# Performance work log

Hardware: AMD Instinct MI355X
Metric: run time of the kernel (lower is better)

The kernel has to match this reference:

```python
import jax, jax.numpy as jnp
import numpy as np

H = 256          # hidden_size
TH_X = 0.05      # delta threshold on inputs
TH_H = 0.05      # delta threshold on hidden state
F_IN = 6         # engineered feature count


def hardswish(v):
    return v * jnp.clip(v + 3.0, 0.0, 6.0) / 6.0


def setup_inputs() -> dict:
    key = jax.random.key(0)
    ks = jax.random.split(key, 6)
    B, T = 32, 4096
    x = jax.random.normal(ks[0], (B, T, 2), dtype=jnp.float32)
    # x2h: Linear(6, 3H, bias=False) -> weight (3H, 6)
    Wx = jax.random.normal(ks[1], (3 * H, F_IN), dtype=jnp.float32) * (1.0 / np.sqrt(F_IN))
    # h2h: Linear(H, 3H, bias=False) -> weight (3H, H)
    Wh = jax.random.normal(ks[2], (3 * H, H), dtype=jnp.float32) * (1.0 / np.sqrt(H))
    # fc_out: Linear(H, 2, bias=False)
    Wo = jax.random.normal(ks[3], (2, H), dtype=jnp.float32) * (1.0 / np.sqrt(H))
    # tcn conv1: Conv1d(2, 3, k=3, padding=16, dilation=16, bias=False) -> (O,I,K)=(3,2,3)
    Wc1 = jax.random.normal(ks[4], (3, 2, 3), dtype=jnp.float32) * 0.3
    # tcn conv2: Conv1d(3, 2, k=1) -> (2,3,1)
    Wc2 = jax.random.normal(ks[5], (2, 3, 1), dtype=jnp.float32) * 0.3
    return {"x": x, "Wx": Wx, "Wh": Wh, "Wo": Wo, "Wc1": Wc1, "Wc2": Wc2}


def _delta_gru(feats_TBF, Wx, Wh):
    # feats_TBF: (T, B, 6). Initial states are always zeros (the torch module
    # resets them whenever x_p_0 is None, which DeltaGRUModel always passes).
    T, B, F = feats_TBF.shape
    dt = feats_TBF.dtype
    carry0 = (
        jnp.zeros((B, F), dt),        # x_p
        jnp.zeros((B, H), dt),        # h
        jnp.zeros((B, H), dt),        # h_p
        jnp.zeros((B, H), dt),        # dm_nh
        jnp.zeros((B, 3 * H), dt),    # dm
    )

    def step(carry, xt):
        x_p, h, h_p, dm_nh, dm = carry
        dx = xt - x_p
        dh = h - h_p
        dxa = jnp.abs(dx)
        dha = jnp.abs(dh)
        dx = jnp.where(dxa < TH_X, 0.0, dx)
        dh = jnp.where(dha < TH_H, 0.0, dh)
        x_p = jnp.where(dxa >= TH_X, xt, x_p)
        h_p = jnp.where(dha >= TH_H, h, h_p)
        mac_x = dx @ Wx.T + dm          # (B, 3H)
        mac_h = dh @ Wh.T               # (B, 3H)
        mxr, mxz, mxn = jnp.split(mac_x, 3, axis=1)
        mhr, mhz, mhn = jnp.split(mac_h, 3, axis=1)
        dm_r = mxr + mhr
        dm_z = mxz + mhz
        dm_n = mxn
        dm_nh = mhn + dm_nh
        dm = jnp.concatenate([dm_r, dm_z, dm_n], axis=1)
        r = jax.nn.sigmoid(dm_r)
        z = jax.nn.sigmoid(dm_z)
        n = jnp.tanh(dm_n + r * dm_nh)
        h = (1.0 - z) * n + z * h
        return (x_p, h, h_p, dm_nh, dm), h

    _, hs = jax.lax.scan(step, carry0, feats_TBF)  # hs: (T, B, H)
    return hs


def reference(x, Wx, Wh, Wo, Wc1, Wc2):
    # x: (B, T, 2)
    B, T, _ = x.shape
    # --- TCN skip path ---
    xc = jnp.transpose(x, (0, 2, 1))  # (B, 2, T)
    c1 = jax.lax.conv_general_dilated(
        xc, Wc1, window_strides=(1,), padding=[(16, 16)], rhs_dilation=(16,),
        dimension_numbers=("NCH", "OIH", "NCH"))
    c2 = jax.lax.conv_general_dilated(
        hardswish(c1), Wc2, window_strides=(1,), padding=[(0, 0)],
        dimension_numbers=("NCH", "OIH", "NCH"))
    skip = jnp.transpose(hardswish(c2), (0, 2, 1))  # (B, T, 2)
    # --- engineered features ---
    i = x[..., 0:1]
    q = x[..., 1:2]
    amp2 = i * i + q * q
    amp = jnp.sqrt(jnp.maximum(amp2, 1e-12))
    amp3 = amp * amp2
    i_prev = jnp.pad(i[:, :-1, :], ((0, 0), (1, 0), (0, 0)))
    q_prev = jnp.pad(q[:, :-1, :], ((0, 0), (1, 0), (0, 0)))
    feats = jnp.concatenate([i, q, amp, amp3, i_prev, q_prev], axis=-1)  # (B,T,6)
    # --- delta-GRU scan (time-major) ---
    hs = _delta_gru(jnp.transpose(feats, (1, 0, 2)), Wx, Wh)  # (T, B, H)
    out = jnp.transpose(hs, (1, 0, 2))  # (B, T, H)
    return out @ Wo.T + skip  # (B, T, 2)
```

## Files before the change

### kernel.cpp

```cpp
#include <hip/hip_runtime.h>
#include <math.h>

#define HH 256
#define FIN 6
#define TT 4096
#define BB 32
#define TH 0.05f

typedef _Float16 h2 __attribute__((ext_vector_type(2)));
struct __align__(16) H8 { h2 a, b, c, d; };

__device__ __forceinline__ float hswish(float v) {
    float c = fminf(fmaxf(v + 3.0f, 0.0f), 6.0f);
    return v * c * (1.0f / 6.0f);
}
__device__ __forceinline__ float fexp2(float x) { return __builtin_amdgcn_exp2f(x); }
__device__ __forceinline__ float frcp(float x)  { return __builtin_amdgcn_rcpf(x); }
__device__ __forceinline__ float sigm(float x)  { return frcp(1.0f + fexp2(-1.44269504f * x)); }
__device__ __forceinline__ float tanhf_fast(float x) {
    float ax = fabsf(x);
    float e = fexp2(2.88539008f * ax);
    float t = 1.0f - 2.0f * frcp(e + 1.0f);
    return copysignf(t, x);
}

__device__ __forceinline__ float dpp_row_sum16(float p) {
    int x = __float_as_int(p);
    p += __int_as_float(__builtin_amdgcn_update_dpp(0, x, 0x118, 0xF, 0xF, true));
    x = __float_as_int(p);
    p += __int_as_float(__builtin_amdgcn_update_dpp(0, x, 0x114, 0xF, 0xF, true));
    x = __float_as_int(p);
    p += __int_as_float(__builtin_amdgcn_update_dpp(0, x, 0x112, 0xF, 0xF, true));
    x = __float_as_int(p);
    p += __int_as_float(__builtin_amdgcn_update_dpp(0, x, 0x111, 0xF, 0xF, true));
    return p;
}

__global__ __launch_bounds__(256) void k_prep(
        const float* __restrict__ x, const float* __restrict__ Wc1,
        const float* __restrict__ Wc2, float* __restrict__ feats,
        float* __restrict__ out) {
    int idx = blockIdx.x * 256 + threadIdx.x;
    if (idx >= BB * TT) return;
    int b = idx >> 12;
    int t = idx & (TT - 1);
    const float* xb = x + (size_t)b * TT * 2;
    float i0 = xb[t * 2 + 0], q0 = xb[t * 2 + 1];
    float ip = (t > 0) ? xb[(t - 1) * 2 + 0] : 0.0f;
    float qp = (t > 0) ? xb[(t - 1) * 2 + 1] : 0.0f;
    float amp2 = i0 * i0 + q0 * q0;
    float amp  = sqrtf(fmaxf(amp2, 1e-12f));
    float amp3 = amp * amp2;
    float* f = feats + (size_t)idx * 6;
    f[0] = i0; f[1] = q0; f[2] = amp; f[3] = amp3; f[4] = ip; f[5] = qp;

    float c1[3];
#pragma unroll
    for (int m = 0; m < 3; m++) {
        float acc = 0.0f;
#pragma unroll
        for (int k = 0; k < 3; k++) {
            int tt = t + (k - 1) * 16;
            if (tt >= 0 && tt < TT) {
                acc += Wc1[m * 6 + 0 * 3 + k] * xb[tt * 2 + 0];
                acc += Wc1[m * 6 + 1 * 3 + k] * xb[tt * 2 + 1];
            }
        }
        c1[m] = hswish(acc);
    }
#pragma unroll
    for (int o = 0; o < 2; o++) {
        float acc = Wc2[o * 3 + 0] * c1[0] + Wc2[o * 3 + 1] * c1[1] + Wc2[o * 3 + 2] * c1[2];
        out[(size_t)idx * 2 + o] = hswish(acc);
    }
}

__global__ __launch_bounds__(256) void k_pack(
        const float* __restrict__ Wh, _Float16* __restrict__ zp,
        _Float16* __restrict__ np) {
    int id = blockIdx.x * 256 + threadIdx.x;
    if (id >= 16384) return;
    int which = id >> 13;
    int c     = (id >> 9) & 15;
    int slice = id & 511;
    int row = slice & 255, half = slice >> 8;
    int g = 1 + which;
    const float* src = Wh + ((size_t)(g * HH + row)) * HH + half * 128 + 8 * c;
    _Float16* dst = (which ? np : zp) + ((size_t)c * 512 + slice) * 8;
#pragma unroll
    for (int j = 0; j < 8; j++) dst[j] = (_Float16)src[j];
}

#define CH(CC, NR) { H8 zw_ = zl[(CC) * 512]; H8 dd_ = dp[CC];                 \
    ar0 = __builtin_amdgcn_fdot2(dd_.a, wr[4 * (CC) + 0], ar0, false);         \
    az0 = __builtin_amdgcn_fdot2(dd_.a, zw_.a, az0, false);                    \
    an0 = __builtin_amdgcn_fdot2(dd_.a, NR.a, an0, false);                     \
    ar1 = __builtin_amdgcn_fdot2(dd_.b, wr[4 * (CC) + 1], ar1, false);         \
    az1 = __builtin_amdgcn_fdot2(dd_.b, zw_.b, az1, false);                    \
    an1 = __builtin_amdgcn_fdot2(dd_.b, NR.b, an1, false);                     \
    ar0 = __builtin_amdgcn_fdot2(dd_.c, wr[4 * (CC) + 2], ar0, false);         \
    az0 = __builtin_amdgcn_fdot2(dd_.c, zw_.c, az0, false);                    \
    an0 = __builtin_amdgcn_fdot2(dd_.c, NR.c, an0, false);                     \
    ar1 = __builtin_amdgcn_fdot2(dd_.d, wr[4 * (CC) + 3], ar1, false);         \
    az1 = __builtin_amdgcn_fdot2(dd_.d, zw_.d, az1, false);                    \
    an1 = __builtin_amdgcn_fdot2(dd_.d, NR.d, an1, false); }

__global__ __launch_bounds__(512) void k_gru(
        const float* __restrict__ feats, const float* __restrict__ Wx,
        const float* __restrict__ Wh, const float* __restrict__ Wo,
        const _Float16* __restrict__ zp, const _Float16* __restrict__ np,
        float* __restrict__ out) {
    extern __shared__ __align__(16) _Float16 z_lds[];
    __shared__ __align__(16) _Float16 s_dhh[2][HH];
    __shared__ __align__(16) float s_dx[2][8];

    const int tid  = threadIdx.x;
    const int wv   = tid >> 6;
    const int lane = tid & 63;
    const int half = lane >> 5;
    const int row  = wv * 32 + (lane & 31);
    const int slice = half * 256 + row;
    const int b    = blockIdx.x;
    const float* fb = feats + (size_t)b * TT * FIN;
    float* outb = out + (size_t)b * TT * 2;

    for (int i = tid; i < 8192; i += 512)
        ((float4*)z_lds)[i] = ((const float4*)zp)[i];

    h2 wr[64];
    {
        const float4* p0 = (const float4*)(Wh + (size_t)(0 * HH + row) * HH + half * 128);
#pragma unroll
        for (int c = 0; c < 32; c++) {
            float4 v0 = p0[c];
            wr[2 * c]     = h2{(_Float16)v0.x, (_Float16)v0.y};
            wr[2 * c + 1] = h2{(_Float16)v0.z, (_Float16)v0.w};
        }
    }
    float wxr0, wxr1, wxr2, wxz0, wxz1, wxz2, wxn0, wxn1, wxn2;
    {
        const int f0 = 3 * half;
        wxr0 = Wx[(size_t)(0 * HH + row) * FIN + f0];
        wxr1 = Wx[(size_t)(0 * HH + row) * FIN + f0 + 1];
        wxr2 = Wx[(size_t)(0 * HH + row) * FIN + f0 + 2];
        wxz0 = Wx[(size_t)(1 * HH + row) * FIN + f0];
        wxz1 = Wx[(size_t)(1 * HH + row) * FIN + f0 + 1];
        wxz2 = Wx[(size_t)(1 * HH + row) * FIN + f0 + 2];
        wxn0 = Wx[(size_t)(2 * HH + row) * FIN + f0];
        wxn1 = Wx[(size_t)(2 * HH + row) * FIN + f0 + 1];
        wxn2 = Wx[(size_t)(2 * HH + row) * FIN + f0 + 2];
    }
    const float woc = Wo[half * HH + row];

    float h = 0.0f, hp = 0.0f, dmr = 0.0f, dmz = 0.0f, dmn = 0.0f, dmnh = 0.0f;
    float xp = 0.0f, curf = 0.0f;
    if (tid < FIN) curf = fb[tid];

    const H8* zl = (const H8*)z_lds + slice;
    const H8* nl = (const H8*)np + slice;

    __syncthreads();

    for (int t = 0; t < TT; t++) {
        const int tb = t & 1;

        {
            float dh = h - hp;
            bool keep = fabsf(dh) >= TH;
            if (half == 0) s_dhh[tb][row] = (_Float16)(keep ? dh : 0.0f);
            if (keep) hp = h;
        }
        if (tid < FIN) {
            float dx = curf - xp;
            bool keep = fabsf(dx) >= TH;
            s_dx[tb][tid] = keep ? dx : 0.0f;
            if (keep) xp = curf;
        }
        __syncthreads();

        float dxa = s_dx[tb][3 * half], dxb = s_dx[tb][3 * half + 1],
              dxc = s_dx[tb][3 * half + 2];
        float ar0 = fmaf(dxa, wxr0, fmaf(dxb, wxr1, dxc * wxr2));
        float az0 = fmaf(dxa, wxz0, fmaf(dxb, wxz1, dxc * wxz2));
        float axn = fmaf(dxa, wxn0, fmaf(dxb, wxn1, dxc * wxn2));
        float ar1 = 0.0f, az1 = 0.0f, an0 = 0.0f, an1 = 0.0f;

        const H8* dp = (const H8*)s_dhh[tb] + half * 16;
        {
            H8 na0 = nl[0 * 512],  na1 = nl[1 * 512],  na2 = nl[2 * 512],  na3 = nl[3 * 512];
            H8 nb0 = nl[4 * 512],  nb1 = nl[5 * 512],  nb2 = nl[6 * 512],  nb3 = nl[7 * 512];
            CH(0, na0) CH(1, na1) CH(2, na2) CH(3, na3)
            na0 = nl[8 * 512];  na1 = nl[9 * 512];  na2 = nl[10 * 512]; na3 = nl[11 * 512];
            CH(4, nb0) CH(5, nb1) CH(6, nb2) CH(7, nb3)
            nb0 = nl[12 * 512]; nb1 = nl[13 * 512]; nb2 = nl[14 * 512]; nb3 = nl[15 * 512];
            CH(8, na0) CH(9, na1) CH(10, na2) CH(11, na3)
            CH(12, nb0) CH(13, nb1) CH(14, nb2) CH(15, nb3)
        }
        float ar = ar0 + ar1, az = az0 + az1, an = an0 + an1;
        ar  += __shfl_xor(ar, 32, 64);
        az  += __shfl_xor(az, 32, 64);
        an  += __shfl_xor(an, 32, 64);
        axn += __shfl_xor(axn, 32, 64);

        dmr += ar;
        dmz += az;
        dmn += axn;
        dmnh += an;

        {
            float r = sigm(dmr);
            float z = sigm(dmz);
            float nn = tanhf_fast(dmn + r * dmnh);
            h = (1.0f - z) * nn + z * h;
        }

        {
            float p = h * woc;
            p += __shfl_xor(p, 16, 64);
            p = dpp_row_sum16(p);
            if ((lane & 31) == 31) atomicAdd(&outb[2 * t + half], p);
        }

        if (tid < FIN && t + 1 < TT) curf = fb[(size_t)(t + 1) * FIN + tid];
    }
}

extern "C" void kernel_launch(void* const* d_in, const int* in_sizes, int n_in,
                              void* d_out, int out_size, void* d_ws, size_t ws_size,
                              hipStream_t stream) {
    const float* x   = (const float*)d_in[0];
    const float* Wx  = (const float*)d_in[1];
    const float* Wh  = (const float*)d_in[2];
    const float* Wo  = (const float*)d_in[3];
    const float* Wc1 = (const float*)d_in[4];
    const float* Wc2 = (const float*)d_in[5];
    float* out = (float*)d_out;
    float* feats = (float*)d_ws;
    _Float16* zp = (_Float16*)((char*)d_ws + 3145728);
    _Float16* np = (_Float16*)((char*)d_ws + 3145728 + 131072);

    k_prep<<<(BB * TT + 255) / 256, 256, 0, stream>>>(x, Wc1, Wc2, feats, out);
    k_pack<<<64, 256, 0, stream>>>(Wh, zp, np);
    hipFuncSetAttribute(reinterpret_cast<const void*>(k_gru),
                        hipFuncAttributeMaxDynamicSharedMemorySize, 131072);
    k_gru<<<BB, 512, 131072, stream>>>(feats, Wx, Wh, Wo, zp, np, out);
}
```

Measured before the change: 5.169 ms.

## Compute recurrent gate matvecs with MFMA 16x16x32 tiles instead of fdot2

Replaces the per-lane fdot2 dot products for the hidden-to-hidden matvec with MFMA f16 instructions. The dh vector is broadcast as the B operand and the diagonal is extracted from the accumulators. Wh is repacked into MFMA A-operand layout: the r gate stays in registers, z lives in LDS, and n is streamed from global memory with software prefetch. The block shrinks to 256 threads and Wx moves to LDS. This cuts the serial per-step latency, at the cost of wasting most of each MFMA on a matrix-vector product and needing extra select logic to extract the result.

```diff
diff --git a/kernel.cpp b/kernel.cpp
--- a/kernel.cpp
+++ b/kernel.cpp
@@ -7,8 +7,8 @@
 #define BB 32
 #define TH 0.05f
 
-typedef _Float16 h2 __attribute__((ext_vector_type(2)));
-struct __align__(16) H8 { h2 a, b, c, d; };
+typedef _Float16 half8 __attribute__((ext_vector_type(8)));
+typedef float f4 __attribute__((ext_vector_type(4)));
 
 __device__ __forceinline__ float hswish(float v) {
     float c = fminf(fmaxf(v + 3.0f, 0.0f), 6.0f);
@@ -80,132 +80,179 @@
         _Float16* __restrict__ np) {
     int id = blockIdx.x * 256 + threadIdx.x;
     if (id >= 16384) return;
-    int which = id >> 13;
-    int c     = (id >> 9) & 15;
-    int slice = id & 511;
-    int row = slice & 255, half = slice >> 8;
-    int g = 1 + which;
-    const float* src = Wh + ((size_t)(g * HH + row)) * HH + half * 128 + 8 * c;
-    _Float16* dst = (which ? np : zp) + ((size_t)c * 512 + slice) * 8;
-#pragma unroll
-    for (int j = 0; j < 8; j++) dst[j] = (_Float16)src[j];
-}
-
-#define CH(CC, NR) { H8 zw_ = zl[(CC) * 512]; H8 dd_ = dp[CC];                 \
-    ar0 = __builtin_amdgcn_fdot2(dd_.a, wr[4 * (CC) + 0], ar0, false);         \
-    az0 = __builtin_amdgcn_fdot2(dd_.a, zw_.a, az0, false);                    \
-    an0 = __builtin_amdgcn_fdot2(dd_.a, NR.a, an0, false);                     \
-    ar1 = __builtin_amdgcn_fdot2(dd_.b, wr[4 * (CC) + 1], ar1, false);         \
-    az1 = __builtin_amdgcn_fdot2(dd_.b, zw_.b, az1, false);                    \
-    an1 = __builtin_amdgcn_fdot2(dd_.b, NR.b, an1, false);                     \
-    ar0 = __builtin_amdgcn_fdot2(dd_.c, wr[4 * (CC) + 2], ar0, false);         \
-    az0 = __builtin_amdgcn_fdot2(dd_.c, zw_.c, az0, false);                    \
-    an0 = __builtin_amdgcn_fdot2(dd_.c, NR.c, an0, false);                     \
-    ar1 = __builtin_amdgcn_fdot2(dd_.d, wr[4 * (CC) + 3], ar1, false);         \
-    az1 = __builtin_amdgcn_fdot2(dd_.d, zw_.d, az1, false);                    \
-    an1 = __builtin_amdgcn_fdot2(dd_.d, NR.d, an1, false); }
-
-__global__ __launch_bounds__(512) void k_gru(
+    int gi  = id >> 13;
+    int fid = id & 8191;
+    int rt  = fid >> 9;
+    int kc  = (fid >> 6) & 7;
+    int ln  = fid & 63;
+    const float* s = Wh + ((size_t)((1 + gi) * HH + 16 * rt + (ln & 15))) * HH
+                   + 32 * kc + ((ln >> 4) & 3) * 8;
+    _Float16* d = (gi ? np : zp) + (size_t)fid * 8;
+    float4 u = *(const float4*)s;
+    float4 v = *(const float4*)(s + 4);
+    d[0] = (_Float16)u.x; d[1] = (_Float16)u.y; d[2] = (_Float16)u.z; d[3] = (_Float16)u.w;
+    d[4] = (_Float16)v.x; d[5] = (_Float16)v.y; d[6] = (_Float16)v.z; d[7] = (_Float16)v.w;
+}
+
+#define MFMA(A, B, C) __builtin_amdgcn_mfma_f32_16x16x32_f16((A), (B), (C), 0, 0, 0)
+
+#define EXTRACT(C0, C1, C2, C3, DST) {                                         \
+    float e0_ = c2 ? (c1 ? C0[3] : C0[2]) : (c1 ? C0[1] : C0[0]);              \
+    float e1_ = c2 ? (c1 ? C1[3] : C1[2]) : (c1 ? C1[1] : C1[0]);              \
+    float e2_ = c2 ? (c1 ? C2[3] : C2[2]) : (c1 ? C2[1] : C2[0]);              \
+    float e3_ = c2 ? (c1 ? C3[3] : C3[2]) : (c1 ? C3[1] : C3[0]);              \
+    float u0_ = b1t ? e1_ : e0_;                                               \
+    float u1_ = b1t ? e3_ : e2_;                                               \
+    DST = b2t ? u1_ : u0_; }
+
+#define RS(KC) {                                                               \
+    half8 bf = *(const half8*)(dhb + 32 * (KC) + a_ * 8);                      \
+    cr0 = MFMA(ar[0][KC], bf, cr0); cr1 = MFMA(ar[1][KC], bf, cr1);            \
+    cr2 = MFMA(ar[2][KC], bf, cr2); cr3 = MFMA(ar[3][KC], bf, cr3); }
+
+#define ZN(KC, N0, N1, N2, N3) {                                               \
+    half8 bf = *(const half8*)(dhb + 32 * (KC) + a_ * 8);                      \
+    half8 z0 = zlb[o0 + (KC) * 64];                                            \
+    half8 z1 = zlb[o1 + (KC) * 64];                                            \
+    half8 z2 = zlb[o2 + (KC) * 64];                                            \
+    half8 z3 = zlb[o3 + (KC) * 64];                                            \
+    cz0 = MFMA(z0, bf, cz0); cz1 = MFMA(z1, bf, cz1);                          \
+    cz2 = MFMA(z2, bf, cz2); cz3 = MFMA(z3, bf, cz3);                          \
+    cn0 = MFMA(N0, bf, cn0); cn1 = MFMA(N1, bf, cn1);                          \
+    cn2 = MFMA(N2, bf, cn2); cn3 = MFMA(N3, bf, cn3); }
+
+#define NL(P, N0, N1, N2, N3)                                                  \
+    N0 = nlb[o0 + (P) * 64]; N1 = nlb[o1 + (P) * 64];                          \
+    N2 = nlb[o2 + (P) * 64]; N3 = nlb[o3 + (P) * 64];
+
+__global__ __launch_bounds__(256) void k_gru(
         const float* __restrict__ feats, const float* __restrict__ Wx,
         const float* __restrict__ Wh, const float* __restrict__ Wo,
         const _Float16* __restrict__ zp, const _Float16* __restrict__ np,
         float* __restrict__ out) {
-    extern __shared__ __align__(16) _Float16 z_lds[];
-    __shared__ __align__(16) _Float16 s_dhh[2][HH];
-    __shared__ __align__(16) float s_dx[2][8];
+    extern __shared__ __align__(16) char smem[];
+    _Float16* z_lds = (_Float16*)smem;
+    float*    s_wx  = (float*)(smem + 131072);
+    _Float16* s_dhh = (_Float16*)(smem + 131072 + 20480);
+    float*    s_dx  = (float*)(smem + 131072 + 20480 + 1024);
 
     const int tid  = threadIdx.x;
-    const int wv   = tid >> 6;
+    const int w    = tid >> 6;
     const int lane = tid & 63;
-    const int half = lane >> 5;
-    const int row  = wv * 32 + (lane & 31);
-    const int slice = half * 256 + row;
+    const int a_   = (lane >> 4) & 3;
+    const bool c1  = lane & 1, c2 = lane & 2, b1t = lane & 4, b2t = lane & 8;
+    const int rowR = 64 * w + 16 * ((lane >> 2) & 3) + 4 * a_ + (lane & 3);
     const int b    = blockIdx.x;
     const float* fb = feats + (size_t)b * TT * FIN;
     float* outb = out + (size_t)b * TT * 2;
 
-    for (int i = tid; i < 8192; i += 512)
+    for (int i = tid; i < 8192; i += 256)
         ((float4*)z_lds)[i] = ((const float4*)zp)[i];
-
-    h2 wr[64];
-    {
-        const float4* p0 = (const float4*)(Wh + (size_t)(0 * HH + row) * HH + half * 128);
-#pragma unroll
-        for (int c = 0; c < 32; c++) {
-            float4 v0 = p0[c];
-            wr[2 * c]     = h2{(_Float16)v0.x, (_Float16)v0.y};
-            wr[2 * c + 1] = h2{(_Float16)v0.z, (_Float16)v0.w};
-        }
-    }
-    float wxr0, wxr1, wxr2, wxz0, wxz1, wxz2, wxn0, wxn1, wxn2;
-    {
-        const int f0 = 3 * half;
-        wxr0 = Wx[(size_t)(0 * HH + row) * FIN + f0];
-        wxr1 = Wx[(size_t)(0 * HH + row) * FIN + f0 + 1];
-        wxr2 = Wx[(size_t)(0 * HH + row) * FIN + f0 + 2];
-        wxz0 = Wx[(size_t)(1 * HH + row) * FIN + f0];
-        wxz1 = Wx[(size_t)(1 * HH + row) * FIN + f0 + 1];
-        wxz2 = Wx[(size_t)(1 * HH + row) * FIN + f0 + 2];
-        wxn0 = Wx[(size_t)(2 * HH + row) * FIN + f0];
-        wxn1 = Wx[(size_t)(2 * HH + row) * FIN + f0 + 1];
-        wxn2 = Wx[(size_t)(2 * HH + row) * FIN + f0 + 2];
-    }
-    const float woc = Wo[half * HH + row];
+    for (int i = tid; i < 256 * 18; i += 256) {
+        int r = i / 18, gf = i - r * 18;
+        int g = gf / 6, f = gf - g * 6;
+        s_wx[r * 20 + gf] = Wx[((size_t)g * HH + r) * FIN + f];
+    }
+    if (tid < 4) s_dx[(tid >> 1) * 8 + 6 + (tid & 1)] = 0.0f;
+
+    half8 ar[4][8];
+#pragma unroll
+    for (int ti = 0; ti < 4; ti++) {
+#pragma unroll
+        for (int kc = 0; kc < 8; kc++) {
+            const float* q = Wh + ((size_t)(16 * (4 * w + ti) + (lane & 15))) * HH
+                           + 32 * kc + a_ * 8;
+            float4 u = *(const float4*)q;
+            float4 v = *(const float4*)(q + 4);
+            half8 tt;
+            tt[0] = (_Float16)u.x; tt[1] = (_Float16)u.y;
+            tt[2] = (_Float16)u.z; tt[3] = (_Float16)u.w;
+            tt[4] = (_Float16)v.x; tt[5] = (_Float16)v.y;
+            tt[6] = (_Float16)v.z; tt[7] = (_Float16)v.w;
+            ar[ti][kc] = tt;
+        }
+    }
+    const float wo0 = Wo[rowR], wo1 = Wo[HH + rowR];
+
+    const half8* zlb = (const half8*)z_lds;
+    const half8* nlb = (const half8*)np;
+    const int o0 = (4 * w + 0) * 512 + lane;
+    const int o1 = (4 * w + 1) * 512 + lane;
+    const int o2 = (4 * w + 2) * 512 + lane;
+    const int o3 = (4 * w + 3) * 512 + lane;
 
     float h = 0.0f, hp = 0.0f, dmr = 0.0f, dmz = 0.0f, dmn = 0.0f, dmnh = 0.0f;
-    float xp = 0.0f, curf = 0.0f;
+    float xp = 0.0f, curf = 0.0f, curfN = 0.0f;
     if (tid < FIN) curf = fb[tid];
-
-    const H8* zl = (const H8*)z_lds + slice;
-    const H8* nl = (const H8*)np + slice;
 
     __syncthreads();
 
     for (int t = 0; t < TT; t++) {
         const int tb = t & 1;
+        const _Float16* dhb = s_dhh + tb * HH;
 
         {
             float dh = h - hp;
             bool keep = fabsf(dh) >= TH;
-            if (half == 0) s_dhh[tb][row] = (_Float16)(keep ? dh : 0.0f);
+            s_dhh[tb * HH + rowR] = (_Float16)(keep ? dh : 0.0f);
             if (keep) hp = h;
         }
         if (tid < FIN) {
             float dx = curf - xp;
             bool keep = fabsf(dx) >= TH;
-            s_dx[tb][tid] = keep ? dx : 0.0f;
+            s_dx[tb * 8 + tid] = keep ? dx : 0.0f;
             if (keep) xp = curf;
-        }
+            if (t + 1 < TT) curfN = fb[(size_t)(t + 1) * FIN + tid];
+        }
+        half8 nA0, nA1, nA2, nA3, nB0, nB1, nB2, nB3;
+        NL(0, nA0, nA1, nA2, nA3)
+        NL(1, nB0, nB1, nB2, nB3)
+
         __syncthreads();
 
-        float dxa = s_dx[tb][3 * half], dxb = s_dx[tb][3 * half + 1],
-              dxc = s_dx[tb][3 * half + 2];
-        float ar0 = fmaf(dxa, wxr0, fmaf(dxb, wxr1, dxc * wxr2));
-        float az0 = fmaf(dxa, wxz0, fmaf(dxb, wxz1, dxc * wxz2));
-        float axn = fmaf(dxa, wxn0, fmaf(dxb, wxn1, dxc * wxn2));
-        float ar1 = 0.0f, az1 = 0.0f, an0 = 0.0f, an1 = 0.0f;
-
-        const H8* dp = (const H8*)s_dhh[tb] + half * 16;
-        {
-            H8 na0 = nl[0 * 512],  na1 = nl[1 * 512],  na2 = nl[2 * 512],  na3 = nl[3 * 512];
-            H8 nb0 = nl[4 * 512],  nb1 = nl[5 * 512],  nb2 = nl[6 * 512],  nb3 = nl[7 * 512];
-            CH(0, na0) CH(1, na1) CH(2, na2) CH(3, na3)
-            na0 = nl[8 * 512];  na1 = nl[9 * 512];  na2 = nl[10 * 512]; na3 = nl[11 * 512];
-            CH(4, nb0) CH(5, nb1) CH(6, nb2) CH(7, nb3)
-            nb0 = nl[12 * 512]; nb1 = nl[13 * 512]; nb2 = nl[14 * 512]; nb3 = nl[15 * 512];
-            CH(8, na0) CH(9, na1) CH(10, na2) CH(11, na3)
-            CH(12, nb0) CH(13, nb1) CH(14, nb2) CH(15, nb3)
-        }
-        float ar = ar0 + ar1, az = az0 + az1, an = an0 + an1;
-        ar  += __shfl_xor(ar, 32, 64);
-        az  += __shfl_xor(az, 32, 64);
-        an  += __shfl_xor(an, 32, 64);
-        axn += __shfl_xor(axn, 32, 64);
-
-        dmr += ar;
-        dmz += az;
-        dmn += axn;
-        dmnh += an;
+        float mxr, mxz, mxn;
+        {
+            const float4 da = *(const float4*)(s_dx + tb * 8);
+            const float4 db = *(const float4*)(s_dx + tb * 8 + 4);
+            const float4 x0 = *(const float4*)(s_wx + rowR * 20);
+            const float4 x1 = *(const float4*)(s_wx + rowR * 20 + 4);
+            const float4 x2 = *(const float4*)(s_wx + rowR * 20 + 8);
+            const float4 x3 = *(const float4*)(s_wx + rowR * 20 + 12);
+            const float4 x4 = *(const float4*)(s_wx + rowR * 20 + 16);
+            mxr = fmaf(da.x, x0.x, fmaf(da.y, x0.y, fmaf(da.z, x0.z,
+                  fmaf(da.w, x0.w, fmaf(db.x, x1.x, db.y * x1.y)))));
+            mxz = fmaf(da.x, x1.z, fmaf(da.y, x1.w, fmaf(da.z, x2.x,
+                  fmaf(da.w, x2.y, fmaf(db.x, x2.z, db.y * x2.w)))));
+            mxn = fmaf(da.x, x3.x, fmaf(da.y, x3.y, fmaf(da.z, x3.z,
+                  fmaf(da.w, x3.w, fmaf(db.x, x4.x, db.y * x4.y)))));
+        }
+
+        f4 cr0 = {0.f,0.f,0.f,0.f}, cr1 = {0.f,0.f,0.f,0.f};
+        f4 cr2 = {0.f,0.f,0.f,0.f}, cr3 = {0.f,0.f,0.f,0.f};
+        RS(0) RS(1) RS(2) RS(3) RS(4) RS(5) RS(6) RS(7)
+        float arv;
+        EXTRACT(cr0, cr1, cr2, cr3, arv)
+
+        f4 cz0 = {0.f,0.f,0.f,0.f}, cz1 = {0.f,0.f,0.f,0.f};
+        f4 cz2 = {0.f,0.f,0.f,0.f}, cz3 = {0.f,0.f,0.f,0.f};
+        f4 cn0 = {0.f,0.f,0.f,0.f}, cn1 = {0.f,0.f,0.f,0.f};
+        f4 cn2 = {0.f,0.f,0.f,0.f}, cn3 = {0.f,0.f,0.f,0.f};
+        ZN(0, nA0, nA1, nA2, nA3)  NL(2, nA0, nA1, nA2, nA3)
+        ZN(1, nB0, nB1, nB2, nB3)  NL(3, nB0, nB1, nB2, nB3)
+        ZN(2, nA0, nA1, nA2, nA3)  NL(4, nA0, nA1, nA2, nA3)
+        ZN(3, nB0, nB1, nB2, nB3)  NL(5, nB0, nB1, nB2, nB3)
+        ZN(4, nA0, nA1, nA2, nA3)  NL(6, nA0, nA1, nA2, nA3)
+        ZN(5, nB0, nB1, nB2, nB3)  NL(7, nB0, nB1, nB2, nB3)
+        ZN(6, nA0, nA1, nA2, nA3)
+        ZN(7, nB0, nB1, nB2, nB3)
+        float azv, anv;
+        EXTRACT(cz0, cz1, cz2, cz3, azv)
+        EXTRACT(cn0, cn1, cn2, cn3, anv)
+
+        dmr += mxr + arv;
+        dmz += mxz + azv;
+        dmn += mxn;
+        dmnh += anv;
 
         {
             float r = sigm(dmr);
@@ -215,13 +262,16 @@
         }
 
         {
-            float p = h * woc;
-            p += __shfl_xor(p, 16, 64);
-            p = dpp_row_sum16(p);
-            if ((lane & 31) == 31) atomicAdd(&outb[2 * t + half], p);
-        }
-
-        if (tid < FIN && t + 1 < TT) curf = fb[(size_t)(t + 1) * FIN + tid];
+            float p0 = h * wo0, p1 = h * wo1;
+            p0 += __shfl_xor(p0, 16, 64); p0 += __shfl_xor(p0, 32, 64);
+            p0 = dpp_row_sum16(p0);
+            p1 += __shfl_xor(p1, 16, 64); p1 += __shfl_xor(p1, 32, 64);
+            p1 = dpp_row_sum16(p1);
+            if (lane == 15) atomicAdd(&outb[2 * t + 0], p0);
+            if (lane == 31) atomicAdd(&outb[2 * t + 1], p1);
+        }
+
+        curf = curfN;
     }
 }
 
@@ -242,6 +292,6 @@
     k_prep<<<(BB * TT + 255) / 256, 256, 0, stream>>>(x, Wc1, Wc2, feats, out);
     k_pack<<<64, 256, 0, stream>>>(Wh, zp, np);
     hipFuncSetAttribute(reinterpret_cast<const void*>(k_gru),
-                        hipFuncAttributeMaxDynamicSharedMemorySize, 131072);
-    k_gru<<<BB, 512, 131072, stream>>>(feats, Wx, Wh, Wo, zp, np, out);
-}
+                        hipFuncAttributeMaxDynamicSharedMemorySize, 152640);
+    k_gru<<<BB, 256, 152640, stream>>>(feats, Wx, Wh, Wo, zp, np, out);
+}
```

New measurement: 8.989 ms. +73.9%, slower.
